# Kernel optimization log

Hardware: AMD Instinct MI355X
Metric: run time of the kernel (lower is better)

## Reference

```python
import jax, jax.numpy as jnp
import numpy as np

B, S, DM, H = 16, 4096, 512, 4
HD = DM // H  # head_dim = 128
EPS = 1e-5


def setup_inputs() -> dict:
    key = jax.random.key(0)
    ks = jax.random.split(key, 9)
    sc = 1.0 / np.sqrt(DM)
    inp = {
        "x": jax.random.normal(ks[0], (B, S, DM), dtype=jnp.float32),
        "Wq_w": jax.random.normal(ks[1], (DM, DM), dtype=jnp.float32) * sc,
        "Wq_b": jnp.zeros((DM,), dtype=jnp.float32),
        "Wk_w": jax.random.normal(ks[2], (DM, DM), dtype=jnp.float32) * sc,
        "Wk_b": jnp.zeros((DM,), dtype=jnp.float32),
        "Wv_w": jax.random.normal(ks[3], (DM, DM), dtype=jnp.float32) * sc,
        "Wv_b": jnp.zeros((DM,), dtype=jnp.float32),
        "Wo_w": jax.random.normal(ks[4], (DM, DM), dtype=jnp.float32) * sc,
        "Wo_b": jnp.zeros((DM,), dtype=jnp.float32),
        "ln_g": jnp.ones((DM,), dtype=jnp.float32),
        "ln_b": jnp.zeros((DM,), dtype=jnp.float32),
    }
    return inp


def _forward(x, Wq_w, Wq_b, Wk_w, Wk_b, Wv_w, Wv_b, Wo_w, Wo_b, ln_g, ln_b):
    b, s, _ = x.shape
    # Linear projections, viewed as [B,S,H,HD] exactly as the torch code does
    Q = (x @ Wq_w.T + Wq_b).reshape(b, s, H, HD)
    K = (x @ Wk_w.T + Wk_b).reshape(b, s, H, HD)
    V = (x @ Wv_w.T + Wv_b).reshape(b, s, H, HD)
    # NOTE: source never permutes heads to dim 1, so attention is over the
    # HEAD axis per token: scores [B,S,H,H]
    scores = jnp.einsum("bshd,bstd->bsht", Q, K) / np.sqrt(HD).astype(np.float32)
    attn = jax.nn.softmax(scores, axis=-1)  # dropout is identity in eval
    out = jnp.einsum("bsht,bstd->bshd", attn, V).reshape(b, s, DM)
    out = out @ Wo_w.T + Wo_b
    y = out + x  # input_dim == output_dim -> residual branch taken
    mu = jnp.mean(y, axis=-1, keepdims=True)
    var = jnp.mean((y - mu) ** 2, axis=-1, keepdims=True)
    return (y - mu) * jax.lax.rsqrt(var + EPS) * ln_g + ln_b


def reference(x, Wq_w, Wq_b, Wk_w, Wk_b, Wv_w, Wv_b, Wo_w, Wo_b, ln_g, ln_b):
    return _forward(x, Wq_w, Wq_b, Wk_w, Wk_b, Wv_w, Wv_b, Wo_w, Wo_b, ln_g, ln_b)
```

## Files before the change

### kernel.cpp

```cpp
#include <hip/hip_runtime.h>
#include <stdint.h>

#define NTOK 65536
#define DMODEL 512
#define QKVN 1536
#define LN_EPS 1e-5f

typedef __attribute__((ext_vector_type(8))) short short8;
typedef __attribute__((ext_vector_type(8))) unsigned short ushort8;
typedef __attribute__((ext_vector_type(4))) float float4_t;
typedef __attribute__((ext_vector_type(4))) unsigned int uint4_t;

static __device__ __forceinline__ float bf2f(unsigned short u) {
    union { unsigned int i; float f; } c; c.i = ((unsigned int)u) << 16; return c.f;
}
static __device__ __forceinline__ unsigned short f2bf(float f) {
    union { float f; unsigned int i; } c; c.f = f;
    unsigned int x = c.i;
    return (unsigned short)((x + 0x7fffu + ((x >> 16) & 1u)) >> 16);
}
static __device__ __forceinline__ unsigned int cvt_pk_bf16(float lo, float hi) {
    unsigned int r;
    asm("v_cvt_pk_bf16_f32 %0, %1, %2" : "=v"(r) : "v"(lo), "v"(hi));
    return r;
}
static __device__ __forceinline__ void gload_lds16(const void* g, void* l) {
    __builtin_amdgcn_global_load_lds((const __attribute__((address_space(1))) void*)g,
                                     (__attribute__((address_space(3))) void*)l, 16, 0, 0);
}

#define BAR() __builtin_amdgcn_s_barrier()
#define WAITL0() asm volatile("s_waitcnt lgkmcnt(0)" ::: "memory")
#define WVM(n) asm volatile("s_waitcnt vmcnt(" #n ")" ::: "memory")
#define MFMA(a, b, c) __builtin_amdgcn_mfma_f32_16x16x32_bf16((a), (b), (c), 0, 0, 0)

__global__ __launch_bounds__(256) void cast_x_kernel(const float* __restrict__ x,
                                                     unsigned short* __restrict__ xb, int n8) {
    int stride = gridDim.x * blockDim.x;
#pragma unroll 2
    for (int i = blockIdx.x * blockDim.x + threadIdx.x; i < n8; i += stride) {
        const float4_t* p = (const float4_t*)(x + (size_t)i * 8);
        float4_t a = p[0], b = p[1];
        ushort8 v;
        v[0] = f2bf(a[0]); v[1] = f2bf(a[1]); v[2] = f2bf(a[2]); v[3] = f2bf(a[3]);
        v[4] = f2bf(b[0]); v[5] = f2bf(b[1]); v[6] = f2bf(b[2]); v[7] = f2bf(b[3]);
        *(ushort8*)(xb + (size_t)i * 8) = v;
    }
}

__global__ __launch_bounds__(256) void prep_w_kernel(
    const float* __restrict__ wq, const float* __restrict__ wk, const float* __restrict__ wv,
    const float* __restrict__ wo,
    const float* __restrict__ bq, const float* __restrict__ bk, const float* __restrict__ bv,
    unsigned short* __restrict__ wqkv, unsigned short* __restrict__ wpack,
    float* __restrict__ bias_qkv) {
    const int WN = DMODEL * DMODEL;
    int tid = blockIdx.x * blockDim.x + threadIdx.x;
    int stride = gridDim.x * blockDim.x;
    for (int j = tid; j < 3 * WN; j += stride) {
        int seg = j / WN, idx = j - seg * WN;
        const float* src = (seg == 0) ? wq : (seg == 1) ? wk : wv;
        wqkv[j] = f2bf(src[idx]);
    }
    for (int j = tid; j < WN; j += stride) {
        int e = j & 7, l = (j >> 3) & 63, nf = (j >> 9) & 31, kt = j >> 14;
        int row = nf * 16 + (l & 15);
        int k = kt * 32 + ((l >> 4) << 3) + e;
        wpack[j] = f2bf(wo[row * 512 + k]);
    }
    for (int j = tid; j < QKVN; j += stride)
        bias_qkv[j] = (j < 512) ? bq[j] : (j < 1024) ? bk[j - 512] : bv[j - 1024];
}

__global__ __launch_bounds__(512, 2) void gemm1_kernel(
    const unsigned short* __restrict__ A, const unsigned short* __restrict__ Bw,
    const float* __restrict__ bias, unsigned short* __restrict__ Cout) {
    __shared__ unsigned short As[4][256 * 32];
    __shared__ unsigned short Bs[4][256 * 32];

    const int b = blockIdx.x;
    const int L = (b & 7) * 192 + (b >> 3);
    const int bm = L / 6;
    const int bn = L - bm * 6;

    const int t = threadIdx.x;
    const int lane = t & 63;
    const int w = t >> 6;
    const int wm = w >> 2, wn = w & 3;

    const unsigned short* Ab = A + (size_t)bm * 256 * 512;
    const unsigned short* Bb = Bw + (size_t)bn * 256 * 512;

    const int i0 = t, i1 = 512 + t;
    const int r0 = i0 >> 2, s0 = (i0 & 3) ^ ((r0 >> 1) & 3);
    const int r1 = i1 >> 2, s1 = (i1 & 3) ^ ((r1 >> 1) & 3);

#define STAGE_A1(kt) do { \
        gload_lds16(Ab + r0 * 512 + (kt) * 32 + s0 * 8, &As[(kt) & 3][i0 * 8]); \
        gload_lds16(Ab + r1 * 512 + (kt) * 32 + s1 * 8, &As[(kt) & 3][i1 * 8]); } while (0)
#define STAGE_B1(kt) do { \
        gload_lds16(Bb + r0 * 512 + (kt) * 32 + s0 * 8, &Bs[(kt) & 3][i0 * 8]); \
        gload_lds16(Bb + r1 * 512 + (kt) * 32 + s1 * 8, &Bs[(kt) & 3][i1 * 8]); } while (0)

    int aoff[8], boff[4];
#pragma unroll
    for (int m = 0; m < 8; m++) {
        int row = wm * 128 + m * 16 + (lane & 15);
        aoff[m] = row * 32 + (((lane >> 4) ^ ((row >> 1) & 3)) * 8);
    }
#pragma unroll
    for (int n = 0; n < 4; n++) {
        int row = wn * 64 + n * 16 + (lane & 15);
        boff[n] = row * 32 + (((lane >> 4) ^ ((row >> 1) & 3)) * 8);
    }

    float4_t acc[8][4];
#pragma unroll
    for (int m = 0; m < 8; m++)
#pragma unroll
        for (int n = 0; n < 4; n++) acc[m][n] = (float4_t){0.f, 0.f, 0.f, 0.f};

    STAGE_A1(0); STAGE_B1(0);
    STAGE_A1(1); STAGE_B1(1);
    STAGE_A1(2); STAGE_B1(2);
    WVM(8);
    BAR();

    short8 ar[8], br[4];
#pragma unroll
    for (int kt = 0; kt < 16; ++kt) {
        const int sl = kt & 3;
#pragma unroll
        for (int m = 0; m < 8; m++) ar[m] = *(const short8*)&As[sl][aoff[m]];
        br[0] = *(const short8*)&Bs[sl][boff[0]];
        br[1] = *(const short8*)&Bs[sl][boff[1]];
        if (kt <= 12) STAGE_A1(kt + 3);
        BAR();
        WAITL0();
        __builtin_amdgcn_s_setprio(1);
#pragma unroll
        for (int m = 0; m < 8; m++) {
            acc[m][0] = MFMA(ar[m], br[0], acc[m][0]);
            acc[m][1] = MFMA(ar[m], br[1], acc[m][1]);
        }
        __builtin_amdgcn_s_setprio(0);
        BAR();
        br[2] = *(const short8*)&Bs[sl][boff[2]];
        br[3] = *(const short8*)&Bs[sl][boff[3]];
        if (kt <= 12) STAGE_B1(kt + 3);
        BAR();
        WAITL0();
        __builtin_amdgcn_s_setprio(1);
#pragma unroll
        for (int m = 0; m < 8; m++) {
            acc[m][2] = MFMA(ar[m], br[2], acc[m][2]);
            acc[m][3] = MFMA(ar[m], br[3], acc[m][3]);
        }
        __builtin_amdgcn_s_setprio(0);
        if (kt <= 12) { WVM(8); }
        else if (kt == 13) { WVM(4); }
        else if (kt == 14) { WVM(0); }
        BAR();
    }

    const int orow0 = bm * 256 + wm * 128;
    const int ocol0 = bn * 256 + wn * 64;
#pragma unroll
    for (int m = 0; m < 8; m++) {
#pragma unroll
        for (int n = 0; n < 4; n++) {
            int col = ocol0 + n * 16 + (lane & 15);
            float bv = bias[col];
#pragma unroll
            for (int j = 0; j < 4; j++) {
                int row = orow0 + m * 16 + (lane >> 4) * 4 + j;
                Cout[(size_t)row * QKVN + col] = f2bf(acc[m][n][j] + bv);
            }
        }
    }
#undef STAGE_A1
#undef STAGE_B1
}

__global__ __launch_bounds__(256, 2) void attn_o_ln_kernel(
    const unsigned short* __restrict__ qkv, const unsigned short* __restrict__ Wpack,
    const float* __restrict__ bo, const float* __restrict__ xres,
    const float* __restrict__ lng, const float* __restrict__ lnb,
    float* __restrict__ Y) {
    __shared__ __align__(16) unsigned char QKVs[49152];
    __shared__ __align__(16) unsigned char AOs[16384];
    float* red = (float*)QKVs;

    const int T0 = blockIdx.x * 16;
    const int t = threadIdx.x;
    const int lane = t & 63;
    const int w = t >> 6;
    const int g = lane >> 4;
    const int sl = lane & 15;

#pragma unroll
    for (int j = 0; j < 12; j++) {
        const int row = w * 4 + j / 3;
        const int part = j % 3;
        gload_lds16(qkv + (size_t)(T0 + row) * QKVN + part * 512 + lane * 8,
                    QKVs + row * 3072 + part * 1024 + lane * 16);
    }
    WVM(0);

    const unsigned short* Bb2 = Wpack + ((size_t)(w * 8) * 64 + lane) * 8;
    short8 bA[8], bB[8];
#pragma unroll
    for (int n = 0; n < 8; n++) bA[n] = *(const short8*)(Bb2 + n * 512);
#pragma unroll
    for (int n = 0; n < 8; n++) bB[n] = *(const short8*)(Bb2 + 16384 + n * 512);

    const float scale = 0.08838834764831845f;
    {
        const int tr = w * 4 + g;
        const unsigned char* base = QKVs + tr * 3072 + sl * 16;

#pragma unroll
        for (int h = 0; h < 4; h++) {
            short8 qr = *(const short8*)(base + h * 256);
            float qf[8];
#pragma unroll
            for (int d = 0; d < 8; d++) qf[d] = bf2f((unsigned short)qr[d]);
            float s[4];
#pragma unroll
            for (int tt = 0; tt < 4; tt++) {
                short8 kr = *(const short8*)(base + 1024 + tt * 256);
                float a0 = 0.f;
#pragma unroll
                for (int d = 0; d < 8; d++) a0 += qf[d] * bf2f((unsigned short)kr[d]);
                s[tt] = a0;
            }
#pragma unroll
            for (int mask = 1; mask < 16; mask <<= 1)
#pragma unroll
                for (int tt = 0; tt < 4; tt++)
                    s[tt] += __shfl_xor(s[tt], mask, 64);
            float m0 = fmaxf(fmaxf(s[0], s[1]), fmaxf(s[2], s[3])) * scale;
            float p[4];
            float sum = 0.f;
#pragma unroll
            for (int tt = 0; tt < 4; tt++) { p[tt] = __expf(s[tt] * scale - m0); sum += p[tt]; }
            float rr = __frcp_rn(sum);
            float o[8];
#pragma unroll
            for (int d = 0; d < 8; d++) o[d] = 0.f;
#pragma unroll
            for (int tt = 0; tt < 4; tt++) {
                short8 vr = *(const short8*)(base + 2048 + tt * 256);
                float ph = p[tt] * rr;
#pragma unroll
                for (int d = 0; d < 8; d++) o[d] += ph * bf2f((unsigned short)vr[d]);
            }
            uint4_t pk;
            pk[0] = cvt_pk_bf16(o[0], o[1]);
            pk[1] = cvt_pk_bf16(o[2], o[3]);
            pk[2] = cvt_pk_bf16(o[4], o[5]);
            pk[3] = cvt_pk_bf16(o[6], o[7]);
            int off = tr * 1024 + ((h * 256 + sl * 16) ^ ((tr & 7) << 4));
            *(uint4_t*)(AOs + off) = pk;
        }
    }

    float xf[4][8];
    float bias8[8], gc8[8], bc8[8];
#pragma unroll
    for (int n = 0; n < 8; n++) {
        int c = w * 128 + n * 16 + sl;
        bias8[n] = bo[c]; gc8[n] = lng[c]; bc8[n] = lnb[c];
    }
#pragma unroll
    for (int j = 0; j < 4; j++) {
        const float* xr = xres + (size_t)(T0 + g * 4 + j) * 512;
#pragma unroll
        for (int n = 0; n < 8; n++) xf[j][n] = xr[w * 128 + n * 16 + sl];
    }

    __syncthreads();

    const int arow = sl;
    const int aswz = (arow & 7) << 4;

    float4_t acc[8];
#pragma unroll
    for (int n = 0; n < 8; n++) acc[n] = (float4_t){0.f, 0.f, 0.f, 0.f};

#pragma unroll 1
    for (int kt = 0; kt < 16; kt += 2) {
        short8 a0 = *(const short8*)(AOs + arow * 1024 + ((kt * 64 + g * 16) ^ aswz));
#pragma unroll
        for (int n = 0; n < 8; n++) acc[n] = MFMA(a0, bA[n], acc[n]);
        if (kt + 2 < 16) {
#pragma unroll
            for (int n = 0; n < 8; n++)
                bA[n] = *(const short8*)(Bb2 + (size_t)(kt + 2) * 16384 + n * 512);
        }
        short8 a1 = *(const short8*)(AOs + arow * 1024 + (((kt + 1) * 64 + g * 16) ^ aswz));
#pragma unroll
        for (int n = 0; n < 8; n++) acc[n] = MFMA(a1, bB[n], acc[n]);
        if (kt + 3 < 16) {
#pragma unroll
            for (int n = 0; n < 8; n++)
                bB[n] = *(const short8*)(Bb2 + (size_t)(kt + 3) * 16384 + n * 512);
        }
    }
    __syncthreads();

#pragma unroll
    for (int j = 0; j < 4; j++) {
#pragma unroll
        for (int n = 0; n < 8; n++)
            acc[n][j] += bias8[n] + xf[j][n];
    }
#pragma unroll
    for (int j = 0; j < 4; j++) {
        float s = 0.f, s2 = 0.f;
#pragma unroll
        for (int n = 0; n < 8; n++) { float v = acc[n][j]; s += v; s2 += v * v; }
#pragma unroll
        for (int mask = 1; mask < 16; mask <<= 1) {
            s += __shfl_xor(s, mask, 64);
            s2 += __shfl_xor(s2, mask, 64);
        }
        if (sl == 0) {
            int rl = g * 4 + j;
            red[(rl * 4 + w) * 2 + 0] = s;
            red[(rl * 4 + w) * 2 + 1] = s2;
        }
    }
    __syncthreads();
#pragma unroll
    for (int j = 0; j < 4; j++) {
        int rl = g * 4 + j;
        float s = 0.f, s2 = 0.f;
#pragma unroll
        for (int i = 0; i < 4; i++) {
            s += red[(rl * 4 + i) * 2 + 0];
            s2 += red[(rl * 4 + i) * 2 + 1];
        }
        float mu = s * (1.f / 512.f);
        float var = s2 * (1.f / 512.f) - mu * mu;
        float inv = rsqrtf(var + LN_EPS);
        float* yp = Y + (size_t)(T0 + rl) * 512;
#pragma unroll
        for (int n = 0; n < 8; n++) {
            int c = w * 128 + n * 16 + sl;
            yp[c] = (acc[n][j] - mu) * inv * gc8[n] + bc8[n];
        }
    }
}

extern "C" void kernel_launch(void* const* d_in, const int* in_sizes, int n_in,
                              void* d_out, int out_size, void* d_ws, size_t ws_size,
                              hipStream_t stream) {
    const float* x   = (const float*)d_in[0];
    const float* wq  = (const float*)d_in[1];
    const float* bq  = (const float*)d_in[2];
    const float* wk  = (const float*)d_in[3];
    const float* bk  = (const float*)d_in[4];
    const float* wv  = (const float*)d_in[5];
    const float* bv  = (const float*)d_in[6];
    const float* wo  = (const float*)d_in[7];
    const float* bo  = (const float*)d_in[8];
    const float* lng = (const float*)d_in[9];
    const float* lnb = (const float*)d_in[10];

    char* ws = (char*)d_ws;
    unsigned short* Xb    = (unsigned short*)(ws);
    unsigned short* Wqkv  = (unsigned short*)(ws + 67108864);
    unsigned short* Wpack = (unsigned short*)(ws + 68681728);
    float*          Bqkv  = (float*)        (ws + 69206016);
    unsigned short* QKV   = (unsigned short*)(ws + 69212160);
    float* Y = (float*)d_out;

    cast_x_kernel<<<4096, 256, 0, stream>>>(x, Xb, NTOK * 512 / 8);
    prep_w_kernel<<<1024, 256, 0, stream>>>(wq, wk, wv, wo, bq, bk, bv, Wqkv, Wpack, Bqkv);

    gemm1_kernel<<<(NTOK / 256) * (QKVN / 256), 512, 0, stream>>>(Xb, Wqkv, Bqkv, QKV);

    attn_o_ln_kernel<<<NTOK / 16, 256, 0, stream>>>(QKV, Wpack, bo, x, lng, lnb, Y);
}
```

Baseline: 321.2 us.

## Make attention/O-proj/LN kernel persistent with double-buffered QKV prefetch

Each block of the attention + output-projection + layernorm kernel now handles 8 consecutive 16-token tiles instead of one. The QKV tile for the next iteration is loaded asynchronously into a second LDS buffer while the current tile is processed, so load latency overlaps with compute and per-block launch and setup cost is amortized. The price is a larger LDS footprint (two 48 KB buffers) and launch bounds relaxed to one block per SIMD group. That sharply reduces resident waves per CU for what is likely a bandwidth-bound kernel. The grid shrinks to 512 blocks, which can leave load imbalance across CUs.

```diff
diff --git a/kernel.cpp b/kernel.cpp
--- a/kernel.cpp
+++ b/kernel.cpp
@@ -182,175 +182,184 @@
 #undef STAGE_B1
 }
 
-__global__ __launch_bounds__(256, 2) void attn_o_ln_kernel(
+__global__ __launch_bounds__(256, 1) void attn_o_ln_kernel(
     const unsigned short* __restrict__ qkv, const unsigned short* __restrict__ Wpack,
     const float* __restrict__ bo, const float* __restrict__ xres,
     const float* __restrict__ lng, const float* __restrict__ lnb,
     float* __restrict__ Y) {
-    __shared__ __align__(16) unsigned char QKVs[49152];
+    __shared__ __align__(16) unsigned char QKVs[2][49152];
     __shared__ __align__(16) unsigned char AOs[16384];
-    float* red = (float*)QKVs;
-
-    const int T0 = blockIdx.x * 16;
+    __shared__ float red[16 * 4 * 2];
+
     const int t = threadIdx.x;
     const int lane = t & 63;
     const int w = t >> 6;
     const int g = lane >> 4;
     const int sl = lane & 15;
-
-#pragma unroll
-    for (int j = 0; j < 12; j++) {
-        const int row = w * 4 + j / 3;
-        const int part = j % 3;
-        gload_lds16(qkv + (size_t)(T0 + row) * QKVN + part * 512 + lane * 8,
-                    QKVs + row * 3072 + part * 1024 + lane * 16);
-    }
-    WVM(0);
+    const int tile0 = blockIdx.x * 8;
+
+#define STAGE_QKV(bufi, tile) do { _Pragma("unroll") \
+    for (int j_ = 0; j_ < 12; j_++) { \
+        const int row_ = w * 4 + j_ / 3; \
+        const int part_ = j_ % 3; \
+        gload_lds16(qkv + (size_t)((tile) * 16 + row_) * QKVN + part_ * 512 + lane * 8, \
+                    QKVs[bufi] + row_ * 3072 + part_ * 1024 + lane * 16); \
+    } } while (0)
 
     const unsigned short* Bb2 = Wpack + ((size_t)(w * 8) * 64 + lane) * 8;
-    short8 bA[8], bB[8];
-#pragma unroll
-    for (int n = 0; n < 8; n++) bA[n] = *(const short8*)(Bb2 + n * 512);
-#pragma unroll
-    for (int n = 0; n < 8; n++) bB[n] = *(const short8*)(Bb2 + 16384 + n * 512);
-
     const float scale = 0.08838834764831845f;
-    {
-        const int tr = w * 4 + g;
-        const unsigned char* base = QKVs + tr * 3072 + sl * 16;
-
-#pragma unroll
-        for (int h = 0; h < 4; h++) {
-            short8 qr = *(const short8*)(base + h * 256);
-            float qf[8];
-#pragma unroll
-            for (int d = 0; d < 8; d++) qf[d] = bf2f((unsigned short)qr[d]);
-            float s[4];
-#pragma unroll
-            for (int tt = 0; tt < 4; tt++) {
-                short8 kr = *(const short8*)(base + 1024 + tt * 256);
-                float a0 = 0.f;
-#pragma unroll
-                for (int d = 0; d < 8; d++) a0 += qf[d] * bf2f((unsigned short)kr[d]);
-                s[tt] = a0;
-            }
-#pragma unroll
-            for (int mask = 1; mask < 16; mask <<= 1)
-#pragma unroll
-                for (int tt = 0; tt < 4; tt++)
-                    s[tt] += __shfl_xor(s[tt], mask, 64);
-            float m0 = fmaxf(fmaxf(s[0], s[1]), fmaxf(s[2], s[3])) * scale;
-            float p[4];
-            float sum = 0.f;
-#pragma unroll
-            for (int tt = 0; tt < 4; tt++) { p[tt] = __expf(s[tt] * scale - m0); sum += p[tt]; }
-            float rr = __frcp_rn(sum);
-            float o[8];
-#pragma unroll
-            for (int d = 0; d < 8; d++) o[d] = 0.f;
-#pragma unroll
-            for (int tt = 0; tt < 4; tt++) {
-                short8 vr = *(const short8*)(base + 2048 + tt * 256);
-                float ph = p[tt] * rr;
-#pragma unroll
-                for (int d = 0; d < 8; d++) o[d] += ph * bf2f((unsigned short)vr[d]);
-            }
-            uint4_t pk;
-            pk[0] = cvt_pk_bf16(o[0], o[1]);
-            pk[1] = cvt_pk_bf16(o[2], o[3]);
-            pk[2] = cvt_pk_bf16(o[4], o[5]);
-            pk[3] = cvt_pk_bf16(o[6], o[7]);
-            int off = tr * 1024 + ((h * 256 + sl * 16) ^ ((tr & 7) << 4));
-            *(uint4_t*)(AOs + off) = pk;
-        }
-    }
-
-    float xf[4][8];
+
     float bias8[8], gc8[8], bc8[8];
 #pragma unroll
     for (int n = 0; n < 8; n++) {
         int c = w * 128 + n * 16 + sl;
         bias8[n] = bo[c]; gc8[n] = lng[c]; bc8[n] = lnb[c];
     }
-#pragma unroll
-    for (int j = 0; j < 4; j++) {
-        const float* xr = xres + (size_t)(T0 + g * 4 + j) * 512;
-#pragma unroll
-        for (int n = 0; n < 8; n++) xf[j][n] = xr[w * 128 + n * 16 + sl];
-    }
-
-    __syncthreads();
-
-    const int arow = sl;
-    const int aswz = (arow & 7) << 4;
-
-    float4_t acc[8];
-#pragma unroll
-    for (int n = 0; n < 8; n++) acc[n] = (float4_t){0.f, 0.f, 0.f, 0.f};
+
+    STAGE_QKV(0, tile0);
 
 #pragma unroll 1
-    for (int kt = 0; kt < 16; kt += 2) {
-        short8 a0 = *(const short8*)(AOs + arow * 1024 + ((kt * 64 + g * 16) ^ aswz));
-#pragma unroll
-        for (int n = 0; n < 8; n++) acc[n] = MFMA(a0, bA[n], acc[n]);
-        if (kt + 2 < 16) {
+    for (int it = 0; it < 8; ++it) {
+        const int tile = tile0 + it;
+        const int T0 = tile * 16;
+        const int cur = it & 1;
+
+        if (it < 7) { STAGE_QKV(cur ^ 1, tile + 1); WVM(12); }
+        else        { WVM(0); }
+
+        short8 bA[8], bB[8];
+#pragma unroll
+        for (int n = 0; n < 8; n++) bA[n] = *(const short8*)(Bb2 + n * 512);
+#pragma unroll
+        for (int n = 0; n < 8; n++) bB[n] = *(const short8*)(Bb2 + 16384 + n * 512);
+        float xf[4][8];
+#pragma unroll
+        for (int j = 0; j < 4; j++) {
+            const float* xr = xres + (size_t)(T0 + g * 4 + j) * 512;
+#pragma unroll
+            for (int n = 0; n < 8; n++) xf[j][n] = xr[w * 128 + n * 16 + sl];
+        }
+
+        {
+            const int tr = w * 4 + g;
+            const unsigned char* base = QKVs[cur] + tr * 3072 + sl * 16;
+#pragma unroll
+            for (int h = 0; h < 4; h++) {
+                short8 qr = *(const short8*)(base + h * 256);
+                float qf[8];
+#pragma unroll
+                for (int d = 0; d < 8; d++) qf[d] = bf2f((unsigned short)qr[d]);
+                float s[4];
+#pragma unroll
+                for (int tt = 0; tt < 4; tt++) {
+                    short8 kr = *(const short8*)(base + 1024 + tt * 256);
+                    float a0 = 0.f;
+#pragma unroll
+                    for (int d = 0; d < 8; d++) a0 += qf[d] * bf2f((unsigned short)kr[d]);
+                    s[tt] = a0;
+                }
+#pragma unroll
+                for (int mask = 1; mask < 16; mask <<= 1)
+#pragma unroll
+                    for (int tt = 0; tt < 4; tt++)
+                        s[tt] += __shfl_xor(s[tt], mask, 64);
+                float m0 = fmaxf(fmaxf(s[0], s[1]), fmaxf(s[2], s[3])) * scale;
+                float p[4];
+                float sum = 0.f;
+#pragma unroll
+                for (int tt = 0; tt < 4; tt++) { p[tt] = __expf(s[tt] * scale - m0); sum += p[tt]; }
+                float rr = __frcp_rn(sum);
+                float o[8];
+#pragma unroll
+                for (int d = 0; d < 8; d++) o[d] = 0.f;
+#pragma unroll
+                for (int tt = 0; tt < 4; tt++) {
+                    short8 vr = *(const short8*)(base + 2048 + tt * 256);
+                    float ph = p[tt] * rr;
+#pragma unroll
+                    for (int d = 0; d < 8; d++) o[d] += ph * bf2f((unsigned short)vr[d]);
+                }
+                uint4_t pk;
+                pk[0] = cvt_pk_bf16(o[0], o[1]);
+                pk[1] = cvt_pk_bf16(o[2], o[3]);
+                pk[2] = cvt_pk_bf16(o[4], o[5]);
+                pk[3] = cvt_pk_bf16(o[6], o[7]);
+                int off = tr * 1024 + ((h * 256 + sl * 16) ^ ((tr & 7) << 4));
+                *(uint4_t*)(AOs + off) = pk;
+            }
+        }
+        __syncthreads();
+
+        const int arow = sl;
+        const int aswz = (arow & 7) << 4;
+        float4_t acc[8];
+#pragma unroll
+        for (int n = 0; n < 8; n++) acc[n] = (float4_t){0.f, 0.f, 0.f, 0.f};
+
+#pragma unroll 1
+        for (int kt = 0; kt < 16; kt += 2) {
+            short8 a0 = *(const short8*)(AOs + arow * 1024 + ((kt * 64 + g * 16) ^ aswz));
+#pragma unroll
+            for (int n = 0; n < 8; n++) acc[n] = MFMA(a0, bA[n], acc[n]);
+            if (kt + 2 < 16) {
+#pragma unroll
+                for (int n = 0; n < 8; n++)
+                    bA[n] = *(const short8*)(Bb2 + (size_t)(kt + 2) * 16384 + n * 512);
+            }
+            short8 a1 = *(const short8*)(AOs + arow * 1024 + (((kt + 1) * 64 + g * 16) ^ aswz));
+#pragma unroll
+            for (int n = 0; n < 8; n++) acc[n] = MFMA(a1, bB[n], acc[n]);
+            if (kt + 3 < 16) {
+#pragma unroll
+                for (int n = 0; n < 8; n++)
+                    bB[n] = *(const short8*)(Bb2 + (size_t)(kt + 3) * 16384 + n * 512);
+            }
+        }
+
+#pragma unroll
+        for (int j = 0; j < 4; j++)
 #pragma unroll
             for (int n = 0; n < 8; n++)
-                bA[n] = *(const short8*)(Bb2 + (size_t)(kt + 2) * 16384 + n * 512);
-        }
-        short8 a1 = *(const short8*)(AOs + arow * 1024 + (((kt + 1) * 64 + g * 16) ^ aswz));
-#pragma unroll
-        for (int n = 0; n < 8; n++) acc[n] = MFMA(a1, bB[n], acc[n]);
-        if (kt + 3 < 16) {
-#pragma unroll
-            for (int n = 0; n < 8; n++)
-                bB[n] = *(const short8*)(Bb2 + (size_t)(kt + 3) * 16384 + n * 512);
-        }
-    }
-    __syncthreads();
-
-#pragma unroll
-    for (int j = 0; j < 4; j++) {
-#pragma unroll
-        for (int n = 0; n < 8; n++)
-            acc[n][j] += bias8[n] + xf[j][n];
-    }
-#pragma unroll
-    for (int j = 0; j < 4; j++) {
-        float s = 0.f, s2 = 0.f;
-#pragma unroll
-        for (int n = 0; n < 8; n++) { float v = acc[n][j]; s += v; s2 += v * v; }
-#pragma unroll
-        for (int mask = 1; mask < 16; mask <<= 1) {
-            s += __shfl_xor(s, mask, 64);
-            s2 += __shfl_xor(s2, mask, 64);
-        }
-        if (sl == 0) {
+                acc[n][j] += bias8[n] + xf[j][n];
+
+#pragma unroll
+        for (int j = 0; j < 4; j++) {
+            float s = 0.f, s2 = 0.f;
+#pragma unroll
+            for (int n = 0; n < 8; n++) { float v = acc[n][j]; s += v; s2 += v * v; }
+#pragma unroll
+            for (int mask = 1; mask < 16; mask <<= 1) {
+                s += __shfl_xor(s, mask, 64);
+                s2 += __shfl_xor(s2, mask, 64);
+            }
+            if (sl == 0) {
+                int rl = g * 4 + j;
+                red[(rl * 4 + w) * 2 + 0] = s;
+                red[(rl * 4 + w) * 2 + 1] = s2;
+            }
+        }
+        __syncthreads();
+#pragma unroll
+        for (int j = 0; j < 4; j++) {
             int rl = g * 4 + j;
-            red[(rl * 4 + w) * 2 + 0] = s;
-            red[(rl * 4 + w) * 2 + 1] = s2;
-        }
-    }
-    __syncthreads();
-#pragma unroll
-    for (int j = 0; j < 4; j++) {
-        int rl = g * 4 + j;
-        float s = 0.f, s2 = 0.f;
-#pragma unroll
-        for (int i = 0; i < 4; i++) {
-            s += red[(rl * 4 + i) * 2 + 0];
-            s2 += red[(rl * 4 + i) * 2 + 1];
-        }
-        float mu = s * (1.f / 512.f);
-        float var = s2 * (1.f / 512.f) - mu * mu;
-        float inv = rsqrtf(var + LN_EPS);
-        float* yp = Y + (size_t)(T0 + rl) * 512;
-#pragma unroll
-        for (int n = 0; n < 8; n++) {
-            int c = w * 128 + n * 16 + sl;
-            yp[c] = (acc[n][j] - mu) * inv * gc8[n] + bc8[n];
-        }
-    }
+            float s = 0.f, s2 = 0.f;
+#pragma unroll
+            for (int i = 0; i < 4; i++) {
+                s += red[(rl * 4 + i) * 2 + 0];
+                s2 += red[(rl * 4 + i) * 2 + 1];
+            }
+            float mu = s * (1.f / 512.f);
+            float var = s2 * (1.f / 512.f) - mu * mu;
+            float inv = rsqrtf(var + LN_EPS);
+            float* yp = Y + (size_t)(T0 + rl) * 512;
+#pragma unroll
+            for (int n = 0; n < 8; n++) {
+                int c = w * 128 + n * 16 + sl;
+                yp[c] = (acc[n][j] - mu) * inv * gc8[n] + bc8[n];
+            }
+        }
+    }
+#undef STAGE_QKV
 }
 
 extern "C" void kernel_launch(void* const* d_in, const int* in_sizes, int n_in,
@@ -381,5 +390,5 @@
 
     gemm1_kernel<<<(NTOK / 256) * (QKVN / 256), 512, 0, stream>>>(Xb, Wqkv, Bqkv, QKV);
 
-    attn_o_ln_kernel<<<NTOK / 16, 256, 0, stream>>>(QKV, Wpack, bo, x, lng, lnb, Y);
-}
+    attn_o_ln_kernel<<<512, 256, 0, stream>>>(QKV, Wpack, bo, x, lng, lnb, Y);
+}
```

Result: slower. 377.7 us (+17.6%).

## Process two token tiles per block and prefetch second tile's QKV into registers

Applied to the files above, without the earlier changes.

The attention/O-proj/LayerNorm kernel now handles 32 tokens per block as two 16-token tiles, with half as many blocks. While the first tile's attention runs, the second tile's QKV rows are loaded from global memory into registers, then written to shared memory, hiding part of the load latency. The LayerNorm reduction buffer gets its own shared array, so one barrier can go, and the residual reads move to after the GEMM. In exchange, register pressure rises from 48 extra VGPRs, which may cause spills, and each tile reloads the Wo fragments.

```diff
diff --git a/kernel.cpp b/kernel.cpp
--- a/kernel.cpp
+++ b/kernel.cpp
@@ -189,36 +189,55 @@
     float* __restrict__ Y) {
     __shared__ __align__(16) unsigned char QKVs[49152];
     __shared__ __align__(16) unsigned char AOs[16384];
-    float* red = (float*)QKVs;
-
-    const int T0 = blockIdx.x * 16;
+    __shared__ float red[16 * 4 * 2];
+
     const int t = threadIdx.x;
     const int lane = t & 63;
     const int w = t >> 6;
     const int g = lane >> 4;
     const int sl = lane & 15;
+    const int T0A = blockIdx.x * 32;
+    const int T0B = T0A + 16;
+
+    const unsigned short* Bb2 = Wpack + ((size_t)(w * 8) * 64 + lane) * 8;
+    const float scale = 0.08838834764831845f;
 
 #pragma unroll
     for (int j = 0; j < 12; j++) {
         const int row = w * 4 + j / 3;
         const int part = j % 3;
-        gload_lds16(qkv + (size_t)(T0 + row) * QKVN + part * 512 + lane * 8,
+        gload_lds16(qkv + (size_t)(T0A + row) * QKVN + part * 512 + lane * 8,
                     QKVs + row * 3072 + part * 1024 + lane * 16);
     }
     WVM(0);
 
-    const unsigned short* Bb2 = Wpack + ((size_t)(w * 8) * 64 + lane) * 8;
+    short8 qv1[12];
+#pragma unroll
+    for (int j = 0; j < 12; j++) {
+        const int row = w * 4 + j / 3;
+        const int part = j % 3;
+        qv1[j] = *(const short8*)(qkv + (size_t)(T0B + row) * QKVN + part * 512 + lane * 8);
+    }
+
     short8 bA[8], bB[8];
 #pragma unroll
     for (int n = 0; n < 8; n++) bA[n] = *(const short8*)(Bb2 + n * 512);
 #pragma unroll
     for (int n = 0; n < 8; n++) bB[n] = *(const short8*)(Bb2 + 16384 + n * 512);
 
-    const float scale = 0.08838834764831845f;
+    float bias8[8], gc8[8], bc8[8];
+#pragma unroll
+    for (int n = 0; n < 8; n++) {
+        int c = w * 128 + n * 16 + sl;
+        bias8[n] = bo[c]; gc8[n] = lng[c]; bc8[n] = lnb[c];
+    }
+
+    const int arow = sl;
+    const int aswz = (arow & 7) << 4;
+
     {
         const int tr = w * 4 + g;
         const unsigned char* base = QKVs + tr * 3072 + sl * 16;
-
 #pragma unroll
         for (int h = 0; h < 4; h++) {
             short8 qr = *(const short8*)(base + h * 256);
@@ -265,29 +284,18 @@
         }
     }
 
-    float xf[4][8];
-    float bias8[8], gc8[8], bc8[8];
-#pragma unroll
-    for (int n = 0; n < 8; n++) {
-        int c = w * 128 + n * 16 + sl;
-        bias8[n] = bo[c]; gc8[n] = lng[c]; bc8[n] = lnb[c];
-    }
-#pragma unroll
-    for (int j = 0; j < 4; j++) {
-        const float* xr = xres + (size_t)(T0 + g * 4 + j) * 512;
-#pragma unroll
-        for (int n = 0; n < 8; n++) xf[j][n] = xr[w * 128 + n * 16 + sl];
+#pragma unroll
+    for (int j = 0; j < 12; j++) {
+        const int row = w * 4 + j / 3;
+        const int part = j % 3;
+        *(short8*)(QKVs + row * 3072 + part * 1024 + lane * 16) = qv1[j];
     }
 
     __syncthreads();
 
-    const int arow = sl;
-    const int aswz = (arow & 7) << 4;
-
     float4_t acc[8];
 #pragma unroll
     for (int n = 0; n < 8; n++) acc[n] = (float4_t){0.f, 0.f, 0.f, 0.f};
-
 #pragma unroll 1
     for (int kt = 0; kt < 16; kt += 2) {
         short8 a0 = *(const short8*)(AOs + arow * 1024 + ((kt * 64 + g * 16) ^ aswz));
@@ -307,13 +315,13 @@
                 bB[n] = *(const short8*)(Bb2 + (size_t)(kt + 3) * 16384 + n * 512);
         }
     }
-    __syncthreads();
 
 #pragma unroll
     for (int j = 0; j < 4; j++) {
+        const float* xr = xres + (size_t)(T0A + g * 4 + j) * 512;
 #pragma unroll
         for (int n = 0; n < 8; n++)
-            acc[n][j] += bias8[n] + xf[j][n];
+            acc[n][j] += bias8[n] + xr[w * 128 + n * 16 + sl];
     }
 #pragma unroll
     for (int j = 0; j < 4; j++) {
@@ -344,7 +352,128 @@
         float mu = s * (1.f / 512.f);
         float var = s2 * (1.f / 512.f) - mu * mu;
         float inv = rsqrtf(var + LN_EPS);
-        float* yp = Y + (size_t)(T0 + rl) * 512;
+        float* yp = Y + (size_t)(T0A + rl) * 512;
+#pragma unroll
+        for (int n = 0; n < 8; n++) {
+            int c = w * 128 + n * 16 + sl;
+            yp[c] = (acc[n][j] - mu) * inv * gc8[n] + bc8[n];
+        }
+    }
+
+#pragma unroll
+    for (int n = 0; n < 8; n++) bA[n] = *(const short8*)(Bb2 + n * 512);
+#pragma unroll
+    for (int n = 0; n < 8; n++) bB[n] = *(const short8*)(Bb2 + 16384 + n * 512);
+
+    {
+        const int tr = w * 4 + g;
+        const unsigned char* base = QKVs + tr * 3072 + sl * 16;
+#pragma unroll
+        for (int h = 0; h < 4; h++) {
+            short8 qr = *(const short8*)(base + h * 256);
+            float qf[8];
+#pragma unroll
+            for (int d = 0; d < 8; d++) qf[d] = bf2f((unsigned short)qr[d]);
+            float s[4];
+#pragma unroll
+            for (int tt = 0; tt < 4; tt++) {
+                short8 kr = *(const short8*)(base + 1024 + tt * 256);
+                float a0 = 0.f;
+#pragma unroll
+                for (int d = 0; d < 8; d++) a0 += qf[d] * bf2f((unsigned short)kr[d]);
+                s[tt] = a0;
+            }
+#pragma unroll
+            for (int mask = 1; mask < 16; mask <<= 1)
+#pragma unroll
+                for (int tt = 0; tt < 4; tt++)
+                    s[tt] += __shfl_xor(s[tt], mask, 64);
+            float m0 = fmaxf(fmaxf(s[0], s[1]), fmaxf(s[2], s[3])) * scale;
+            float p[4];
+            float sum = 0.f;
+#pragma unroll
+            for (int tt = 0; tt < 4; tt++) { p[tt] = __expf(s[tt] * scale - m0); sum += p[tt]; }
+            float rr = __frcp_rn(sum);
+            float o[8];
+#pragma unroll
+            for (int d = 0; d < 8; d++) o[d] = 0.f;
+#pragma unroll
+            for (int tt = 0; tt < 4; tt++) {
+                short8 vr = *(const short8*)(base + 2048 + tt * 256);
+                float ph = p[tt] * rr;
+#pragma unroll
+                for (int d = 0; d < 8; d++) o[d] += ph * bf2f((unsigned short)vr[d]);
+            }
+            uint4_t pk;
+            pk[0] = cvt_pk_bf16(o[0], o[1]);
+            pk[1] = cvt_pk_bf16(o[2], o[3]);
+            pk[2] = cvt_pk_bf16(o[4], o[5]);
+            pk[3] = cvt_pk_bf16(o[6], o[7]);
+            int off = tr * 1024 + ((h * 256 + sl * 16) ^ ((tr & 7) << 4));
+            *(uint4_t*)(AOs + off) = pk;
+        }
+    }
+    __syncthreads();
+
+#pragma unroll
+    for (int n = 0; n < 8; n++) acc[n] = (float4_t){0.f, 0.f, 0.f, 0.f};
+#pragma unroll 1
+    for (int kt = 0; kt < 16; kt += 2) {
+        short8 a0 = *(const short8*)(AOs + arow * 1024 + ((kt * 64 + g * 16) ^ aswz));
+#pragma unroll
+        for (int n = 0; n < 8; n++) acc[n] = MFMA(a0, bA[n], acc[n]);
+        if (kt + 2 < 16) {
+#pragma unroll
+            for (int n = 0; n < 8; n++)
+                bA[n] = *(const short8*)(Bb2 + (size_t)(kt + 2) * 16384 + n * 512);
+        }
+        short8 a1 = *(const short8*)(AOs + arow * 1024 + (((kt + 1) * 64 + g * 16) ^ aswz));
+#pragma unroll
+        for (int n = 0; n < 8; n++) acc[n] = MFMA(a1, bB[n], acc[n]);
+        if (kt + 3 < 16) {
+#pragma unroll
+            for (int n = 0; n < 8; n++)
+                bB[n] = *(const short8*)(Bb2 + (size_t)(kt + 3) * 16384 + n * 512);
+        }
+    }
+
+#pragma unroll
+    for (int j = 0; j < 4; j++) {
+        const float* xr = xres + (size_t)(T0B + g * 4 + j) * 512;
+#pragma unroll
+        for (int n = 0; n < 8; n++)
+            acc[n][j] += bias8[n] + xr[w * 128 + n * 16 + sl];
+    }
+#pragma unroll
+    for (int j = 0; j < 4; j++) {
+        float s = 0.f, s2 = 0.f;
+#pragma unroll
+        for (int n = 0; n < 8; n++) { float v = acc[n][j]; s += v; s2 += v * v; }
+#pragma unroll
+        for (int mask = 1; mask < 16; mask <<= 1) {
+            s += __shfl_xor(s, mask, 64);
+            s2 += __shfl_xor(s2, mask, 64);
+        }
+        if (sl == 0) {
+            int rl = g * 4 + j;
+            red[(rl * 4 + w) * 2 + 0] = s;
+            red[(rl * 4 + w) * 2 + 1] = s2;
+        }
+    }
+    __syncthreads();
+#pragma unroll
+    for (int j = 0; j < 4; j++) {
+        int rl = g * 4 + j;
+        float s = 0.f, s2 = 0.f;
+#pragma unroll
+        for (int i = 0; i < 4; i++) {
+            s += red[(rl * 4 + i) * 2 + 0];
+            s2 += red[(rl * 4 + i) * 2 + 1];
+        }
+        float mu = s * (1.f / 512.f);
+        float var = s2 * (1.f / 512.f) - mu * mu;
+        float inv = rsqrtf(var + LN_EPS);
+        float* yp = Y + (size_t)(T0B + rl) * 512;
 #pragma unroll
         for (int n = 0; n < 8; n++) {
             int c = w * 128 + n * 16 + sl;
@@ -381,5 +510,5 @@
 
     gemm1_kernel<<<(NTOK / 256) * (QKVN / 256), 512, 0, stream>>>(Xb, Wqkv, Bqkv, QKV);
 
-    attn_o_ln_kernel<<<NTOK / 16, 256, 0, stream>>>(QKV, Wpack, bo, x, lng, lnb, Y);
-}
+    attn_o_ln_kernel<<<NTOK / 32, 256, 0, stream>>>(QKV, Wpack, bo, x, lng, lnb, Y);
+}
```

Result: no change. 323.5 us (+0.7%).
